# Performance work log

Hardware: AMD Instinct MI355X
Metric: run time of the kernel (lower is better)

Reference implementation:

```python
import jax, jax.numpy as jnp
import numpy as np

IMAGE_SIZE = 128
FACES_PER_PIXEL = 4
BLUR_RADIUS = 0.01
EPS = 1e-8


def setup_inputs() -> dict:
    key = jax.random.key(0)
    k1, k2, k3 = jax.random.split(key, 3)
    B, V, F = 2, 2000, 800
    # verts are already projected to screen/NDC space: x,y in [-1,1], z > 0 (depth)
    xy = jax.random.uniform(k1, (B, V, 2), minval=-1.0, maxval=1.0)
    z = jax.random.uniform(k2, (B, V, 1), minval=0.5, maxval=2.5)
    verts = jnp.concatenate([xy, z], axis=-1).astype(jnp.float32)
    faces = jax.random.randint(k3, (F, 3), 0, V)
    return {"verts": verts, "faces": faces}


def _edge(a, b, p):
    # signed parallelogram area of (a -> b -> p), using xy components only
    return (p[..., 0] - a[..., 0]) * (b[..., 1] - a[..., 1]) - (
        p[..., 1] - a[..., 1]) * (b[..., 0] - a[..., 0])


def _seg_dist2(p, a, b):
    # squared distance from point p to segment [a, b] in 2D
    ab = b - a
    pa = p - a
    t = jnp.clip(jnp.sum(pa * ab, -1) / (jnp.sum(ab * ab, -1) + EPS), 0.0, 1.0)
    d = pa - t[..., None] * ab
    return jnp.sum(d * d, -1)


def _rasterize(verts, faces):
    H = W = IMAGE_SIZE
    K = FACES_PER_PIXEL
    B = verts.shape[0]
    fv = verts[:, faces]                      # [B,F,3,3] gather face vertices
    v0, v1, v2 = fv[:, :, 0], fv[:, :, 1], fv[:, :, 2]
    a0 = v0[:, None, :, :2]                   # [B,1,F,2]
    a1 = v1[:, None, :, :2]
    a2 = v2[:, None, :, :2]
    z0 = v0[:, None, :, 2]                    # [B,1,F]
    z1 = v1[:, None, :, 2]
    z2 = v2[:, None, :, 2]
    # pixel centers in NDC, pytorch3d convention: index 0 -> +1, last -> -1
    xs = 1.0 - 2.0 * (jnp.arange(W, dtype=verts.dtype) + 0.5) / W
    ys = 1.0 - 2.0 * (jnp.arange(H, dtype=verts.dtype) + 0.5) / H
    yy, xx = jnp.meshgrid(ys, xs, indexing="ij")
    p = jnp.stack([xx, yy], -1).reshape(1, -1, 1, 2)   # [1,P,1,2], P=H*W

    area = _edge(a0, a1, a2)                  # [B,1,F] signed face area*2
    w0 = _edge(a1, a2, p)                     # [B,P,F]
    w1 = _edge(a2, a0, p)
    w2 = _edge(a0, a1, p)
    denom = jnp.where(jnp.abs(area) > EPS, area,
                      jnp.where(area >= 0, EPS, -EPS))
    b0, b1, b2 = w0 / denom, w1 / denom, w2 / denom
    zpix = b0 * z0 + b1 * z1 + b2 * z2        # [B,P,F] interpolated depth

    inside = (b0 >= 0) & (b1 >= 0) & (b2 >= 0)
    dmin = jnp.minimum(_seg_dist2(p, a0, a1),
                       jnp.minimum(_seg_dist2(p, a1, a2),
                                   _seg_dist2(p, a2, a0)))
    dsign = jnp.where(inside, -dmin, dmin)    # signed squared edge distance

    valid = (inside | (dmin < BLUR_RADIUS)) & (zpix > EPS) & (
        jnp.abs(area) > EPS)
    zcand = jnp.where(valid, zpix, jnp.inf)
    _, idx = jax.lax.top_k(-zcand, K)         # K nearest faces per pixel

    take = lambda x: jnp.take_along_axis(x, idx, axis=-1)
    sel_valid = take(valid)
    pix_to_face = jnp.where(sel_valid, idx, -1)
    zbuf = jnp.where(sel_valid, take(zpix), -1.0)
    bary = jnp.stack([b0, b1, b2], -1)        # [B,P,F,3]
    bsel = jnp.take_along_axis(bary, idx[..., None], axis=2)  # [B,P,K,3]
    bsel = jnp.where(sel_valid[..., None], bsel, -1.0)
    dsel = jnp.where(sel_valid, take(dsign), -1.0)

    return (pix_to_face.reshape(B, H, W, K),
            zbuf.reshape(B, H, W, K),
            bsel.reshape(B, H, W, K, 3),
            dsel.reshape(B, H, W, K))


def reference(verts, faces):
    # Fragments: (pix_to_face, zbuf, bary_coords, dists)
    return _rasterize(verts, faces)
```

## Files before the change

kernel.cpp:

```cpp
#include <hip/hip_runtime.h>

#define IMG   128
#define KF    4
#define NF    800
#define NV    2000
#define NB    2
#define EPSF  1e-8f
#define BLURF 0.01f
#define CULL_D2 0.0103f
#define HEXT    0.0547f
#define FARC    0.0102f
#define REC     20

typedef unsigned long long u64;
#define INVK ((((u64)0x7f800000u) << 32) | 0xffffffffu)

#pragma clang fp contract(off)

__device__ __forceinline__ void ins4(u64& s0, u64& s1, u64& s2, u64& s3, u64 k) {
    bool c0 = k < s0, c1 = k < s1, c2 = k < s2, c3 = k < s3;
    s3 = c2 ? s2 : (c3 ? k : s3);
    s2 = c1 ? s1 : (c2 ? k : s2);
    s1 = c0 ? s0 : (c1 ? k : s1);
    s0 = c0 ? k  : s0;
}

__global__ __launch_bounds__(256) void raster_p1(
    const float* __restrict__ verts,
    const int*   __restrict__ faces,
    u64*         __restrict__ part,
    int sh)
{
#pragma clang fp contract(off)
    extern __shared__ float sFD[];
    __shared__ u64 sK[2 * 4 * 64];
    __shared__ unsigned sWc[4];

    const int S     = 1 << sh;
    const int chunk = NF >> sh;
    const int tid   = threadIdx.x;
    const int wave  = tid >> 6;
    const int lane  = tid & 63;
    const int unit  = blockIdx.x;
    const int tile  = unit >> sh;
    const int slice = unit & (S - 1);
    const int b     = tile >> 8;
    const int trow  = (tile & 255) >> 4;
    const int tcol  = tile & 15;
    const float* vb = verts + b * NV * 3;
    const int fbase = slice * chunk;

    const int pr = lane >> 3, pc = lane & 7;
    const int row = trow * 8 + pr, col = tcol * 8 + pc;
    const float px = 1.0f - (2.0f * ((float)col + 0.5f)) / 128.0f;
    const float py = 1.0f - (2.0f * ((float)row + 0.5f)) / 128.0f;
    const float txmax = 1.0f - (2.0f * ((float)(tcol * 8)     + 0.5f)) / 128.0f;
    const float txmin = 1.0f - (2.0f * ((float)(tcol * 8 + 7) + 0.5f)) / 128.0f;
    const float tymax = 1.0f - (2.0f * ((float)(trow * 8)     + 0.5f)) / 128.0f;
    const float tymin = 1.0f - (2.0f * ((float)(trow * 8 + 7) + 0.5f)) / 128.0f;
    const float cx = 0.5f * (txmin + txmax);
    const float cy = 0.5f * (tymin + tymax);

    int scnt = 0;
    for (int j0 = 0; j0 < chunk; j0 += 256) {
        const int jl = j0 + tid;
        bool surv = false;
        float a0x=0,a0y=0,a1x=0,a1y=0,a2x=0,a2y=0,z0=0,z1=0,z2=0,denom=1;
        float e0x=0,e0y=0,e1x=0,e1y=0,e2x=0,e2y=0;
        if (jl < chunk) {
            const int f = fbase + jl;
            int i0 = faces[3*f+0], i1 = faces[3*f+1], i2 = faces[3*f+2];
            a0x = vb[3*i0]; a0y = vb[3*i0+1]; z0 = vb[3*i0+2];
            a1x = vb[3*i1]; a1y = vb[3*i1+1]; z1 = vb[3*i1+2];
            a2x = vb[3*i2]; a2y = vb[3*i2+1]; z2 = vb[3*i2+2];
            float area = (a2x - a0x) * (a1y - a0y) - (a2y - a0y) * (a1x - a0x);
            float aab  = fabsf(area);
            denom = (aab > EPSF) ? area : (area >= 0.0f ? EPSF : -EPSF);
            surv = aab > EPSF;
            float bxmin = fminf(a0x, fminf(a1x, a2x)) - 0.101f;
            float bxmax = fmaxf(a0x, fmaxf(a1x, a2x)) + 0.101f;
            float bymin = fminf(a0y, fminf(a1y, a2y)) - 0.101f;
            float bymax = fmaxf(a0y, fmaxf(a1y, a2y)) + 0.101f;
            surv &= !(bxmin > txmax || bxmax < txmin || bymin > tymax || bymax < tymin);
            float s = (area >= 0.0f) ? 1.0f : -1.0f;
            e0x = a2x - a1x; e0y = a2y - a1y;
            e1x = a0x - a2x; e1y = a0y - a2y;
            e2x = a1x - a0x; e2y = a1y - a0y;
            float w0 = s * ((cx - a1x) * e0y - (cy - a1y) * e0x) + HEXT * (fabsf(e0x) + fabsf(e0y));
            float w1 = s * ((cx - a2x) * e1y - (cy - a2y) * e1x) + HEXT * (fabsf(e1x) + fabsf(e1y));
            float w2 = s * ((cx - a0x) * e2y - (cy - a0y) * e2x) + HEXT * (fabsf(e2x) + fabsf(e2y));
            float l0 = e0x * e0x + e0y * e0y;
            float l1 = e1x * e1x + e1y * e1y;
            float l2 = e2x * e2x + e2y * e2y;
            surv &= !((w0 < 0.0f) & (w0 * w0 > CULL_D2 * l0));
            surv &= !((w1 < 0.0f) & (w1 * w1 > CULL_D2 * l1));
            surv &= !((w2 < 0.0f) & (w2 * w2 > CULL_D2 * l2));
        }
        u64 m = __ballot(surv);
        if (lane == 0) sWc[wave] = (unsigned)__popcll(m);
        __syncthreads();
        int off = scnt;
        for (int w = 0; w < 4; ++w) { if (w < wave) off += (int)sWc[w]; }
        int tot = (int)(sWc[0] + sWc[1] + sWc[2] + sWc[3]);
        if (surv) {
            int pos = off + __popcll(m & ((1ull << lane) - 1ull));
            float* r = &sFD[pos * REC];
            r[0]=a0x; r[1]=a0y; r[2]=a1x; r[3]=a1y; r[4]=a2x; r[5]=a2y;
            r[6]=e0x; r[7]=e0y; r[8]=e1x; r[9]=e1y; r[10]=e2x; r[11]=e2y;
            r[12]=z0; r[13]=z1; r[14]=z2; r[15]=denom;
            r[16] = (e2x * e2x + e2y * e2y) + EPSF;
            r[17] = (e0x * e0x + e0y * e0y) + EPSF;
            r[18] = (e1x * e1x + e1y * e1y) + EPSF;
            r[19] = __int_as_float(fbase + jl);
        }
        scnt += tot;
        __syncthreads();
    }

    u64 s0 = INVK, s1 = INVK, s2 = INVK, s3 = INVK;
    for (int j = wave; j < scnt; j += 4) {
        const float* r = &sFD[j * REC];
        float4 q0 = *(const float4*)(r);
        float4 q1 = *(const float4*)(r + 4);
        float4 q2 = *(const float4*)(r + 8);
        float4 q3 = *(const float4*)(r + 12);
        float4 q4 = *(const float4*)(r + 16);
        float a0x=q0.x, a0y=q0.y, a1x=q0.z, a1y=q0.w, a2x=q1.x, a2y=q1.y;
        float e0x=q1.z, e0y=q1.w, e1x=q2.x, e1y=q2.y, e2x=q2.z, e2y=q2.w;
        float z0=q3.x, z1=q3.y, z2=q3.z, D=q3.w;
        float ddA=q4.x, ddB=q4.y, ddC=q4.z;
        int   fg = __float_as_int(q4.w);
        float p0x = px - a0x, p0y = py - a0y;
        float p1x = px - a1x, p1y = py - a1y;
        float p2x = px - a2x, p2y = py - a2y;
        float w0 = p1x * e0y - p1y * e0x;
        float w1 = p2x * e1y - p2y * e1x;
        float w2 = p0x * e2y - p0y * e2x;
        float b0 = w0 / D, b1 = w1 / D, b2 = w2 / D;
        float zpix = (b0 * z0 + b1 * z1) + b2 * z2;
        bool inside = fminf(b0, fminf(b1, b2)) >= 0.0f;
        bool far = (w0 * w0 > FARC * ddB) & (w1 * w1 > FARC * ddC) & (w2 * w2 > FARC * ddA);
        bool valid;
        if (__all(inside | far)) {
            valid = inside & (zpix > EPSF);
        } else {
            float tA = (p0x * e2x + p0y * e2y) / ddA;
            tA = fminf(fmaxf(tA, 0.0f), 1.0f);
            float dxA = p0x - tA * e2x, dyA = p0y - tA * e2y;
            float dA = dxA * dxA + dyA * dyA;
            float tB = (p1x * e0x + p1y * e0y) / ddB;
            tB = fminf(fmaxf(tB, 0.0f), 1.0f);
            float dxB = p1x - tB * e0x, dyB = p1y - tB * e0y;
            float dB = dxB * dxB + dyB * dyB;
            float tC = (p2x * e1x + p2y * e1y) / ddC;
            tC = fminf(fmaxf(tC, 0.0f), 1.0f);
            float dxC = p2x - tC * e1x, dyC = p2y - tC * e1y;
            float dC = dxC * dxC + dyC * dyC;
            float dmin = fminf(dA, fminf(dB, dC));
            valid = (inside | (dmin < BLURF)) & (zpix > EPSF);
        }
        u64 key = valid ? ((((u64)__float_as_uint(zpix)) << 32) | (unsigned)fg) : INVK;
        if (__any(key < s3)) ins4(s0, s1, s2, s3, key);
    }

    if (wave >= 2) {
        int r = wave - 2;
        sK[(r * 4 + 0) * 64 + lane] = s0;
        sK[(r * 4 + 1) * 64 + lane] = s1;
        sK[(r * 4 + 2) * 64 + lane] = s2;
        sK[(r * 4 + 3) * 64 + lane] = s3;
    }
    __syncthreads();
    if (wave < 2) {
        ins4(s0, s1, s2, s3, sK[(wave * 4 + 0) * 64 + lane]);
        ins4(s0, s1, s2, s3, sK[(wave * 4 + 1) * 64 + lane]);
        ins4(s0, s1, s2, s3, sK[(wave * 4 + 2) * 64 + lane]);
        ins4(s0, s1, s2, s3, sK[(wave * 4 + 3) * 64 + lane]);
    }
    __syncthreads();
    if (wave == 1) {
        sK[0 * 64 + lane] = s0;
        sK[1 * 64 + lane] = s1;
        sK[2 * 64 + lane] = s2;
        sK[3 * 64 + lane] = s3;
    }
    __syncthreads();
    if (wave == 0) {
        ins4(s0, s1, s2, s3, sK[0 * 64 + lane]);
        ins4(s0, s1, s2, s3, sK[1 * 64 + lane]);
        ins4(s0, s1, s2, s3, sK[2 * 64 + lane]);
        ins4(s0, s1, s2, s3, sK[3 * 64 + lane]);
        u64* wrow = part + (size_t)unit * 256;
        wrow[0 * 64 + lane] = s0;
        wrow[1 * 64 + lane] = s1;
        wrow[2 * 64 + lane] = s2;
        wrow[3 * 64 + lane] = s3;
    }
}

__global__ __launch_bounds__(256) void raster_p2(
    const float* __restrict__ verts,
    const int*   __restrict__ faces,
    const u64* __restrict__ part,
    int sh,
    float* __restrict__ out0, float* __restrict__ out1,
    float* __restrict__ out2, float* __restrict__ out3)
{
#pragma clang fp contract(off)
    __shared__ u64 sK[4 * 64];
    const int S    = 1 << sh;
    const int tid  = threadIdx.x;
    const int tile = blockIdx.x;
    const int b    = tile >> 8;
    const int trow = (tile & 255) >> 4;
    const int tcol = tile & 15;
    const float* vb = verts + b * NV * 3;

    if (tid < 64) {
        u64 s0 = INVK, s1 = INVK, s2 = INVK, s3 = INVK;
        const u64* base = part + (size_t)tile * S * 256;
        for (int s = 0; s < S; ++s) {
            ins4(s0, s1, s2, s3, base[s * 256 + 0 * 64 + tid]);
            ins4(s0, s1, s2, s3, base[s * 256 + 1 * 64 + tid]);
            ins4(s0, s1, s2, s3, base[s * 256 + 2 * 64 + tid]);
            ins4(s0, s1, s2, s3, base[s * 256 + 3 * 64 + tid]);
        }
        sK[0 * 64 + tid] = s0;
        sK[1 * 64 + tid] = s1;
        sK[2 * 64 + tid] = s2;
        sK[3 * 64 + tid] = s3;
    }
    __syncthreads();

    int pix = tid >> 2, k = tid & 3;
    u64 key = sK[k * 64 + pix];
    int prow = pix >> 3, pcol = pix & 7;
    int grow = trow * 8 + prow, gcol = tcol * 8 + pcol;
    int p = (b * IMG + grow) * IMG + gcol;
    float qx = 1.0f - (2.0f * ((float)gcol + 0.5f)) / 128.0f;
    float qy = 1.0f - (2.0f * ((float)grow + 0.5f)) / 128.0f;
    float o0 = -1.0f, o1 = -1.0f, ob0 = -1.0f, ob1 = -1.0f, ob2 = -1.0f, o3 = -1.0f;
    if ((unsigned)(key >> 32) != 0x7f800000u) {
        int fi = (int)(unsigned)(key & 0xffffffffu);
        int i0 = faces[3 * fi + 0], i1 = faces[3 * fi + 1], i2 = faces[3 * fi + 2];
        float a0x = vb[3 * i0], a0y = vb[3 * i0 + 1], z0 = vb[3 * i0 + 2];
        float a1x = vb[3 * i1], a1y = vb[3 * i1 + 1], z1 = vb[3 * i1 + 2];
        float a2x = vb[3 * i2], a2y = vb[3 * i2 + 1], z2 = vb[3 * i2 + 2];
        float area = (a2x - a0x) * (a1y - a0y) - (a2y - a0y) * (a1x - a0x);
        float aab  = fabsf(area);
        float denom = (aab > EPSF) ? area : (area >= 0.0f ? EPSF : -EPSF);
        float e0x = a2x - a1x, e0y = a2y - a1y;
        float e1x = a0x - a2x, e1y = a0y - a2y;
        float e2x = a1x - a0x, e2y = a1y - a0y;
        float p0x = qx - a0x, p0y = qy - a0y;
        float p1x = qx - a1x, p1y = qy - a1y;
        float p2x = qx - a2x, p2y = qy - a2y;
        float w0 = p1x * e0y - p1y * e0x;
        float w1 = p2x * e1y - p2y * e1x;
        float w2 = p0x * e2y - p0y * e2x;
        float b0 = w0 / denom, b1 = w1 / denom, b2 = w2 / denom;
        float zpix = (b0 * z0 + b1 * z1) + b2 * z2;
        bool inside = (b0 >= 0.0f) & (b1 >= 0.0f) & (b2 >= 0.0f);
        float ddA = (e2x * e2x + e2y * e2y) + EPSF;
        float tA = (p0x * e2x + p0y * e2y) / ddA;
        tA = fminf(fmaxf(tA, 0.0f), 1.0f);
        float dxA = p0x - tA * e2x, dyA = p0y - tA * e2y;
        float dA = dxA * dxA + dyA * dyA;
        float ddB = (e0x * e0x + e0y * e0y) + EPSF;
        float tB = (p1x * e0x + p1y * e0y) / ddB;
        tB = fminf(fmaxf(tB, 0.0f), 1.0f);
        float dxB = p1x - tB * e0x, dyB = p1y - tB * e0y;
        float dB = dxB * dxB + dyB * dyB;
        float ddC = (e1x * e1x + e1y * e1y) + EPSF;
        float tC = (p2x * e1x + p2y * e1y) / ddC;
        tC = fminf(fmaxf(tC, 0.0f), 1.0f);
        float dxC = p2x - tC * e1x, dyC = p2y - tC * e1y;
        float dC = dxC * dxC + dyC * dyC;
        float dmin = fminf(dA, fminf(dB, dC));
        o0 = (float)fi;
        o1 = zpix;
        ob0 = b0; ob1 = b1; ob2 = b2;
        o3 = inside ? -dmin : dmin;
    }
    int o = p * KF + k;
    out0[o] = o0;
    out1[o] = o1;
    out2[o * 3 + 0] = ob0;
    out2[o * 3 + 1] = ob1;
    out2[o * 3 + 2] = ob2;
    out3[o] = o3;
}

extern "C" void kernel_launch(void* const* d_in, const int* in_sizes, int n_in,
                              void* d_out, int out_size, void* d_ws, size_t ws_size,
                              hipStream_t stream) {
    const float* verts = (const float*)d_in[0];
    const int*   faces = (const int*)d_in[1];
    float* out = (float*)d_out;
    const int n0 = NB * IMG * IMG * KF;

    const size_t per_unit = 256 * sizeof(u64);
    int sh = (ws_size >= (512ull << 3) * per_unit) ? 3 : 2;
    const int S = 1 << sh;
    const int chunk = NF >> sh;
    const size_t dyn = (size_t)chunk * REC * sizeof(float);
    u64* part = (u64*)d_ws;

    raster_p1<<<dim3(512 * S), dim3(256), dyn, stream>>>(verts, faces, part, sh);
    raster_p2<<<dim3(512), dim3(256), 0, stream>>>(verts, faces, part, sh,
        out,
        out + n0,
        out + 2 * n0,
        out + 5 * n0);
}
```

Before: 95.61 us.

## Precompute per-face cull and setup records in a prepass kernel

Adds a prepass kernel that gathers each face's vertices once and writes cull coefficients (bbox plus affine edge functions) and raster records to workspace. The binning kernel now reads these precomputed records, keeps only face indices in shared memory, and fetches full records from global/L2 during shading. The default face split drops from 8 slices to 4, and sh=0 (800-face chunks) is possible when workspace is small. It removes the redundant per-tile vertex gather and setup math, but adds a launch and replaces shared-memory record reads with global loads.

```diff
diff --git a/kernel.cpp b/kernel.cpp
--- a/kernel.cpp
+++ b/kernel.cpp
@@ -10,7 +10,6 @@
 #define CULL_D2 0.0103f
 #define HEXT    0.0547f
 #define FARC    0.0102f
-#define REC     20
 
 typedef unsigned long long u64;
 #define INVK ((((u64)0x7f800000u) << 32) | 0xffffffffu)
@@ -25,14 +24,70 @@
     s0 = c0 ? k  : s0;
 }
 
-__global__ __launch_bounds__(256) void raster_p1(
+__global__ __launch_bounds__(256) void raster_p0(
     const float* __restrict__ verts,
     const int*   __restrict__ faces,
-    u64*         __restrict__ part,
+    float4* __restrict__ cullr,
+    float4* __restrict__ recr)
+{
+#pragma clang fp contract(off)
+    int t = blockIdx.x * 256 + threadIdx.x;
+    if (t >= NB * NF) return;
+    int b = t / NF, f = t - b * NF;
+    const float* vb = verts + b * NV * 3;
+    int i0 = faces[3*f+0], i1 = faces[3*f+1], i2 = faces[3*f+2];
+    float a0x = vb[3*i0], a0y = vb[3*i0+1], z0 = vb[3*i0+2];
+    float a1x = vb[3*i1], a1y = vb[3*i1+1], z1 = vb[3*i1+2];
+    float a2x = vb[3*i2], a2y = vb[3*i2+1], z2 = vb[3*i2+2];
+    float area = (a2x - a0x) * (a1y - a0y) - (a2y - a0y) * (a1x - a0x);
+    float aab  = fabsf(area);
+    float denom = (aab > EPSF) ? area : (area >= 0.0f ? EPSF : -EPSF);
+    float e0x = a2x - a1x, e0y = a2y - a1y;
+    float e1x = a0x - a2x, e1y = a0y - a2y;
+    float e2x = a1x - a0x, e2y = a1y - a0y;
+
+    float4 bb;
+    if (aab > EPSF) {
+        bb.x = fminf(a0x, fminf(a1x, a2x)) - 0.101f;
+        bb.y = fmaxf(a0x, fmaxf(a1x, a2x)) + 0.101f;
+        bb.z = fminf(a0y, fminf(a1y, a2y)) - 0.101f;
+        bb.w = fmaxf(a0y, fmaxf(a1y, a2y)) + 0.101f;
+    } else {
+        bb.x = 1e30f; bb.y = -1e30f; bb.z = 1e30f; bb.w = -1e30f;
+    }
+    float s = (area >= 0.0f) ? 1.0f : -1.0f;
+    float4 E0, E1, E2;
+    E0.x = s * e0y; E0.y = -s * e0x;
+    E0.z = s * (a1y * e0x - a1x * e0y) + HEXT * (fabsf(e0x) + fabsf(e0y));
+    E0.w = CULL_D2 * (e0x * e0x + e0y * e0y);
+    E1.x = s * e1y; E1.y = -s * e1x;
+    E1.z = s * (a2y * e1x - a2x * e1y) + HEXT * (fabsf(e1x) + fabsf(e1y));
+    E1.w = CULL_D2 * (e1x * e1x + e1y * e1y);
+    E2.x = s * e2y; E2.y = -s * e2x;
+    E2.z = s * (a0y * e2x - a0x * e2y) + HEXT * (fabsf(e2x) + fabsf(e2y));
+    E2.w = CULL_D2 * (e2x * e2x + e2y * e2y);
+    float4* cq = &cullr[(size_t)t * 4];
+    cq[0] = bb; cq[1] = E0; cq[2] = E1; cq[3] = E2;
+
+    float4* r = &recr[(size_t)t * 5];
+    r[0] = make_float4(a0x, a0y, a1x, a1y);
+    r[1] = make_float4(a2x, a2y, e0x, e0y);
+    r[2] = make_float4(e1x, e1y, e2x, e2y);
+    r[3] = make_float4(z0, z1, z2, denom);
+    r[4] = make_float4((e2x * e2x + e2y * e2y) + EPSF,
+                       (e0x * e0x + e0y * e0y) + EPSF,
+                       (e1x * e1x + e1y * e1y) + EPSF,
+                       0.0f);
+}
+
+__global__ __launch_bounds__(256) void raster_p1(
+    const float4* __restrict__ cullr,
+    const float4* __restrict__ recr,
+    u64*          __restrict__ part,
     int sh)
 {
 #pragma clang fp contract(off)
-    extern __shared__ float sFD[];
+    __shared__ int sList[800];
     __shared__ u64 sK[2 * 4 * 64];
     __shared__ unsigned sWc[4];
 
@@ -47,7 +102,6 @@
     const int b     = tile >> 8;
     const int trow  = (tile & 255) >> 4;
     const int tcol  = tile & 15;
-    const float* vb = verts + b * NV * 3;
     const int fbase = slice * chunk;
 
     const int pr = lane >> 3, pc = lane & 7;
@@ -65,36 +119,17 @@
     for (int j0 = 0; j0 < chunk; j0 += 256) {
         const int jl = j0 + tid;
         bool surv = false;
-        float a0x=0,a0y=0,a1x=0,a1y=0,a2x=0,a2y=0,z0=0,z1=0,z2=0,denom=1;
-        float e0x=0,e0y=0,e1x=0,e1y=0,e2x=0,e2y=0;
         if (jl < chunk) {
             const int f = fbase + jl;
-            int i0 = faces[3*f+0], i1 = faces[3*f+1], i2 = faces[3*f+2];
-            a0x = vb[3*i0]; a0y = vb[3*i0+1]; z0 = vb[3*i0+2];
-            a1x = vb[3*i1]; a1y = vb[3*i1+1]; z1 = vb[3*i1+2];
-            a2x = vb[3*i2]; a2y = vb[3*i2+1]; z2 = vb[3*i2+2];
-            float area = (a2x - a0x) * (a1y - a0y) - (a2y - a0y) * (a1x - a0x);
-            float aab  = fabsf(area);
-            denom = (aab > EPSF) ? area : (area >= 0.0f ? EPSF : -EPSF);
-            surv = aab > EPSF;
-            float bxmin = fminf(a0x, fminf(a1x, a2x)) - 0.101f;
-            float bxmax = fmaxf(a0x, fmaxf(a1x, a2x)) + 0.101f;
-            float bymin = fminf(a0y, fminf(a1y, a2y)) - 0.101f;
-            float bymax = fmaxf(a0y, fmaxf(a1y, a2y)) + 0.101f;
-            surv &= !(bxmin > txmax || bxmax < txmin || bymin > tymax || bymax < tymin);
-            float s = (area >= 0.0f) ? 1.0f : -1.0f;
-            e0x = a2x - a1x; e0y = a2y - a1y;
-            e1x = a0x - a2x; e1y = a0y - a2y;
-            e2x = a1x - a0x; e2y = a1y - a0y;
-            float w0 = s * ((cx - a1x) * e0y - (cy - a1y) * e0x) + HEXT * (fabsf(e0x) + fabsf(e0y));
-            float w1 = s * ((cx - a2x) * e1y - (cy - a2y) * e1x) + HEXT * (fabsf(e1x) + fabsf(e1y));
-            float w2 = s * ((cx - a0x) * e2y - (cy - a0y) * e2x) + HEXT * (fabsf(e2x) + fabsf(e2y));
-            float l0 = e0x * e0x + e0y * e0y;
-            float l1 = e1x * e1x + e1y * e1y;
-            float l2 = e2x * e2x + e2y * e2y;
-            surv &= !((w0 < 0.0f) & (w0 * w0 > CULL_D2 * l0));
-            surv &= !((w1 < 0.0f) & (w1 * w1 > CULL_D2 * l1));
-            surv &= !((w2 < 0.0f) & (w2 * w2 > CULL_D2 * l2));
+            const float4* cq = &cullr[(size_t)(b * NF + f) * 4];
+            float4 bb = cq[0], E0 = cq[1], E1 = cq[2], E2 = cq[3];
+            surv = !(bb.x > txmax || bb.y < txmin || bb.z > tymax || bb.w < tymin);
+            float w0 = E0.x * cx + E0.y * cy + E0.z;
+            float w1 = E1.x * cx + E1.y * cy + E1.z;
+            float w2 = E2.x * cx + E2.y * cy + E2.z;
+            surv &= !((w0 < 0.0f) & (w0 * w0 > E0.w));
+            surv &= !((w1 < 0.0f) & (w1 * w1 > E1.w));
+            surv &= !((w2 < 0.0f) & (w2 * w2 > E2.w));
         }
         u64 m = __ballot(surv);
         if (lane == 0) sWc[wave] = (unsigned)__popcll(m);
@@ -102,34 +137,20 @@
         int off = scnt;
         for (int w = 0; w < 4; ++w) { if (w < wave) off += (int)sWc[w]; }
         int tot = (int)(sWc[0] + sWc[1] + sWc[2] + sWc[3]);
-        if (surv) {
-            int pos = off + __popcll(m & ((1ull << lane) - 1ull));
-            float* r = &sFD[pos * REC];
-            r[0]=a0x; r[1]=a0y; r[2]=a1x; r[3]=a1y; r[4]=a2x; r[5]=a2y;
-            r[6]=e0x; r[7]=e0y; r[8]=e1x; r[9]=e1y; r[10]=e2x; r[11]=e2y;
-            r[12]=z0; r[13]=z1; r[14]=z2; r[15]=denom;
-            r[16] = (e2x * e2x + e2y * e2y) + EPSF;
-            r[17] = (e0x * e0x + e0y * e0y) + EPSF;
-            r[18] = (e1x * e1x + e1y * e1y) + EPSF;
-            r[19] = __int_as_float(fbase + jl);
-        }
+        if (surv) sList[off + __popcll(m & ((1ull << lane) - 1ull))] = fbase + jl;
         scnt += tot;
         __syncthreads();
     }
 
     u64 s0 = INVK, s1 = INVK, s2 = INVK, s3 = INVK;
     for (int j = wave; j < scnt; j += 4) {
-        const float* r = &sFD[j * REC];
-        float4 q0 = *(const float4*)(r);
-        float4 q1 = *(const float4*)(r + 4);
-        float4 q2 = *(const float4*)(r + 8);
-        float4 q3 = *(const float4*)(r + 12);
-        float4 q4 = *(const float4*)(r + 16);
+        const int fg = sList[j];
+        const float4* r = &recr[(size_t)(b * NF + fg) * 5];
+        float4 q0 = r[0], q1 = r[1], q2 = r[2], q3 = r[3], q4 = r[4];
         float a0x=q0.x, a0y=q0.y, a1x=q0.z, a1y=q0.w, a2x=q1.x, a2y=q1.y;
         float e0x=q1.z, e0y=q1.w, e1x=q2.x, e1y=q2.y, e2x=q2.z, e2y=q2.w;
         float z0=q3.x, z1=q3.y, z2=q3.z, D=q3.w;
         float ddA=q4.x, ddB=q4.y, ddC=q4.z;
-        int   fg = __float_as_int(q4.w);
         float p0x = px - a0x, p0y = py - a0y;
         float p1x = px - a1x, p1y = py - a1y;
         float p2x = px - a2x, p2y = py - a2y;
@@ -299,14 +320,16 @@
     float* out = (float*)d_out;
     const int n0 = NB * IMG * IMG * KF;
 
+    float4* cullr = (float4*)d_ws;
+    float4* recr  = (float4*)((char*)d_ws + 102400);
+    u64*    part  = (u64*)((char*)d_ws + 262144);
+
     const size_t per_unit = 256 * sizeof(u64);
-    int sh = (ws_size >= (512ull << 3) * per_unit) ? 3 : 2;
+    int sh = (ws_size >= 262144 + (512ull << 2) * per_unit) ? 2 : 0;
     const int S = 1 << sh;
-    const int chunk = NF >> sh;
-    const size_t dyn = (size_t)chunk * REC * sizeof(float);
-    u64* part = (u64*)d_ws;
-
-    raster_p1<<<dim3(512 * S), dim3(256), dyn, stream>>>(verts, faces, part, sh);
+
+    raster_p0<<<dim3((NB * NF + 255) / 256), dim3(256), 0, stream>>>(verts, faces, cullr, recr);
+    raster_p1<<<dim3(512 * S), dim3(256), 0, stream>>>(cullr, recr, part, sh);
     raster_p2<<<dim3(512), dim3(256), 0, stream>>>(verts, faces, part, sh,
         out,
         out + n0,
```

Measured after the change: 98.93 us. 3.5% more time.
